# Performance work log

Measured on AMD Instinct MI355X. Metric: run time of the kernel, lower is better.

Reference implementation:

```python
import jax, jax.numpy as jnp
import numpy as np

B, T, C = 4, 2048, 768
H = 12
D = C // H  # head dim 64

def setup_inputs() -> dict:
    key = jax.random.key(0)
    ks = jax.random.split(key, 6)
    scale = 1.0 / np.sqrt(C)
    x = jax.random.normal(ks[0], (B, T, C), dtype=jnp.float32)
    attention_mask = jax.random.randint(ks[1], (B, T), 0, 2, dtype=jnp.int64)
    Wqkv = jax.random.normal(ks[2], (C, 3 * C), dtype=jnp.float32) * scale
    bqkv = jax.random.normal(ks[3], (3 * C,), dtype=jnp.float32) * 0.02
    Wo = jax.random.normal(ks[4], (C, C), dtype=jnp.float32) * scale
    bo = jax.random.normal(ks[5], (C,), dtype=jnp.float32) * 0.02
    return {"x": x, "attention_mask": attention_mask, "Wqkv": Wqkv,
            "bqkv": bqkv, "Wo": Wo, "bo": bo}

def reference(x, attention_mask, Wqkv, bqkv, Wo, bo):
    # fused QKV projection: [B,T,3C]
    qkv = jnp.einsum('btc,cd->btd', x, Wqkv) + bqkv
    q, k, v = jnp.split(qkv, 3, axis=-1)
    # reshape to [B,H,T,D]
    q = q.reshape(B, T, H, D).transpose(0, 2, 1, 3)
    k = k.reshape(B, T, H, D).transpose(0, 2, 1, 3)
    v = v.reshape(B, T, H, D).transpose(0, 2, 1, 3)
    # module quirk: True (attended) where attention_mask == 0
    keep = (attention_mask == 0)[:, None, None, :]  # [B,1,1,T]
    scores = jnp.einsum('bhqd,bhkd->bhqk', q, k) / np.sqrt(D)
    scores = jnp.where(keep, scores, jnp.finfo(scores.dtype).min)
    probs = jax.nn.softmax(scores, axis=-1)
    context = jnp.einsum('bhqk,bhkd->bhqd', probs, v)
    context = context.transpose(0, 2, 1, 3).reshape(B, T, C)
    return jnp.einsum('btc,cd->btd', context, Wo) + bo
```

## Files before the change

### kernel.cpp

```cpp
#include <hip/hip_runtime.h>
#include <stdint.h>

#define AS1 __attribute__((address_space(1)))
#define AS3 __attribute__((address_space(3)))

typedef _Float16 f16;
typedef _Float16 f16x8 __attribute__((ext_vector_type(8)));
typedef _Float16 f16x4 __attribute__((ext_vector_type(4)));
typedef _Float16 f16x2 __attribute__((ext_vector_type(2)));
typedef float    f32x4  __attribute__((ext_vector_type(4)));
typedef float    f32x16 __attribute__((ext_vector_type(16)));
typedef uint32_t u32x4  __attribute__((ext_vector_type(4)));
typedef uint32_t u32x2  __attribute__((ext_vector_type(2)));

#define B_  4
#define T_  2048
#define C_  768
#define H_  12
#define D_  64
#define M_  (B_*T_)
#define N1_ (3*C_)

__device__ __forceinline__ void g2l16(const void* g, void* l) {
  __builtin_amdgcn_global_load_lds((const AS1 void*)g, (AS3 void*)l, 16, 0, 0);
}

__device__ __forceinline__ f32x4 fzero4() { f32x4 z = {0.f, 0.f, 0.f, 0.f}; return z; }

__device__ __forceinline__ uint32_t pk_u32(float a, float b) {
  auto t = __builtin_amdgcn_cvt_pkrtz(a, b);
  return *(uint32_t*)&t;
}

__device__ __forceinline__ void pl32swap(uint32_t& d, uint32_t& s) {
  u32x2 r = __builtin_amdgcn_permlane32_swap(d, s, false, false);
  d = r[0]; s = r[1];
}

__global__ __launch_bounds__(256)
void transpose_cvt_k(const float* __restrict__ in, f16* __restrict__ out, int R, int C) {
  __shared__ float tile[32][33];
  const int tx = threadIdx.x & 31, ty = threadIdx.x >> 5;
  const int c0 = blockIdx.x * 32, r0 = blockIdx.y * 32;
#pragma unroll
  for (int i = 0; i < 32; i += 8)
    tile[ty + i][tx] = in[(long)(r0 + ty + i) * C + c0 + tx];
  __syncthreads();
#pragma unroll
  for (int i = 0; i < 32; i += 8)
    out[(long)(c0 + ty + i) * R + r0 + tx] = (f16)tile[tx][ty + i];
}

__global__ __launch_bounds__(256)
void convert_f32_f16(const float* __restrict__ in, f16* __restrict__ out) {
  const int i = (blockIdx.x * 256 + threadIdx.x) * 4;
  const float4 v = *(const float4*)(in + i);
  f16x4 o = {(f16)v.x, (f16)v.y, (f16)v.z, (f16)v.w};
  *(f16x4*)(out + i) = o;
}

__global__ __launch_bounds__(256)
void init_idx_kernel(int* __restrict__ idx, int* __restrict__ cnt) {
  const int g = blockIdx.x * 256 + threadIdx.x;
  idx[g] = 0;
  if (g < B_) cnt[g] = 0;
}

__global__ __launch_bounds__(256)
void compact_kernel(const int* __restrict__ mask, int* __restrict__ idx,
                    int* __restrict__ cnt) {
  const int b = blockIdx.y;
  const int t = blockIdx.x * 256 + threadIdx.x;
  if (mask[b * T_ + t] == 0) {
    const int s = atomicAdd(&cnt[b], 1);
    idx[b * T_ + s] = t;
  }
}

__global__ __launch_bounds__(256)
void build_vt(const f16* __restrict__ Vc, const int* __restrict__ cnt,
              f16* __restrict__ vt) {
  __shared__ f16 tile[32][33];
  const int z = blockIdx.z, b = z / H_, h = z % H_;
  const int s0 = blockIdx.x * 32, d0 = blockIdx.y * 32;
  if (s0 >= ((cnt[b] + 63) & ~63)) return;
  const int tx = threadIdx.x & 31, ty = threadIdx.x >> 5;
  f16* dst = vt + (long)z * D_ * T_;
#pragma unroll
  for (int i = 0; i < 32; i += 8)
    tile[ty + i][tx] = Vc[(long)(b * T_ + s0 + ty + i) * C_ + h * D_ + d0 + tx];
  __syncthreads();
#pragma unroll
  for (int i = 0; i < 32; i += 8)
    dst[(long)(d0 + ty + i) * T_ + s0 + tx] = tile[tx][ty + i];
}

template <typename OutT>
__global__ __launch_bounds__(256)
void gemm_bias_kernel(const f16* __restrict__ A, const f16* __restrict__ Bt,
                      const float* __restrict__ bias, OutT* __restrict__ Cc,
                      int K, int ldc) {
  __shared__ f16 lA[128 * 32];
  __shared__ f16 lB[128 * 32];
  const int tid = threadIdx.x;
  const int n0 = blockIdx.x * 128, m0 = blockIdx.y * 128;
  const int lane = tid & 63, w = tid >> 6;
  const int wm = (w & 1) * 64, wn = (w >> 1) * 64;
  const int r15 = lane & 15, q4 = lane >> 4;

  const int c0 = tid, c1 = 256 + tid;
  const int ar0 = c0 >> 2, ak0 = (c0 & 3) * 8;
  const int ar1 = c1 >> 2, ak1 = (c1 & 3) * 8;
  const f16* Ab = A + (long)m0 * K;
  const f16* Bb = Bt + (long)n0 * K;

  f32x4 acc[4][4];
#pragma unroll
  for (int i = 0; i < 4; i++)
#pragma unroll
    for (int j = 0; j < 4; j++) acc[i][j] = fzero4();

  for (int kb = 0; kb < K; kb += 32) {
    g2l16(Ab + (long)ar0 * K + kb + ak0, &lA[c0 * 8]);
    g2l16(Ab + (long)ar1 * K + kb + ak1, &lA[c1 * 8]);
    g2l16(Bb + (long)ar0 * K + kb + ak0, &lB[c0 * 8]);
    g2l16(Bb + (long)ar1 * K + kb + ak1, &lB[c1 * 8]);
    __syncthreads();
    f16x8 af[4], bfv[4];
#pragma unroll
    for (int mi = 0; mi < 4; mi++)
      af[mi] = *(const f16x8*)&lA[(wm + mi * 16 + r15) * 32 + q4 * 8];
#pragma unroll
    for (int ni = 0; ni < 4; ni++)
      bfv[ni] = *(const f16x8*)&lB[(wn + ni * 16 + r15) * 32 + q4 * 8];
#pragma unroll
    for (int mi = 0; mi < 4; mi++)
#pragma unroll
      for (int ni = 0; ni < 4; ni++)
        acc[mi][ni] = __builtin_amdgcn_mfma_f32_16x16x32_f16(af[mi], bfv[ni], acc[mi][ni], 0, 0, 0);
    __syncthreads();
  }

#pragma unroll
  for (int ni = 0; ni < 4; ni++) {
    const int col = n0 + wn + ni * 16 + r15;
    const float bs = bias[col];
#pragma unroll
    for (int mi = 0; mi < 4; mi++) {
#pragma unroll
      for (int r = 0; r < 4; r++) {
        const int row = m0 + wm + mi * 16 + q4 * 4 + r;
        Cc[(long)row * ldc + col] = (OutT)(acc[mi][ni][r] + bs);
      }
    }
  }
}

__global__ __launch_bounds__(512, 2)
void gemm_qkv256(const f16* __restrict__ A, const f16* __restrict__ Bt,
                 const float* __restrict__ bias, f16* __restrict__ Qb,
                 f16* __restrict__ Kc, f16* __restrict__ Vc,
                 const int* __restrict__ idx, const int* __restrict__ cnt) {
  const int K = C_;
  __shared__ f16 lA[2 * 256 * 64];
  __shared__ f16 lB[2 * 256 * 64];
  const int tid = threadIdx.x;
  const int nb = blockIdx.x;
  const int mb = blockIdx.y;
  const bool isQ = nb < 3;

  int b = 0, s0 = 0;
  if (!isQ) {
    b = mb >> 3;
    s0 = (mb & 7) * 256;
    if (s0 >= cnt[b]) return;
  }

  const int lane = tid & 63, w = tid >> 6;
  const int wmi = w >> 2, wni = w & 3;
  const int r15 = lane & 15, q4 = lane >> 4;
  const int rx = (r15 & 7) * 8;

  const int trow = tid >> 3;
  const int koffsw = (((tid & 7) ^ (trow & 7)) * 8);
  const f16* pA[4];
  const f16* pB[4];
#pragma unroll
  for (int i = 0; i < 4; i++) {
    const int ri = i * 64 + trow;
    long grow;
    if (isQ) grow = (long)mb * 256 + ri;
    else     grow = (long)b * T_ + idx[b * T_ + s0 + ri];
    pA[i] = A + grow * K + koffsw;
    pB[i] = Bt + (long)(nb * 256 + ri) * K + koffsw;
  }
  const int lofs = tid * 8;

  f32x4 acc[8][4];
#pragma unroll
  for (int i = 0; i < 8; i++)
#pragma unroll
    for (int j = 0; j < 4; j++) acc[i][j] = fzero4();

#define STAGE_QKV(bufsel, kb) do {                                        \
  const int lb = (bufsel) * 16384;                                        \
  _Pragma("unroll")                                                       \
  for (int i = 0; i < 4; i++) {                                           \
    g2l16(pA[i] + (kb), &lA[lb + i * 4096 + lofs]);                       \
    g2l16(pB[i] + (kb), &lB[lb + i * 4096 + lofs]);                       \
  }                                                                       \
} while (0)

#define COMPUTE_QKV(bufsel) do {                                          \
  const int lb = (bufsel) * 16384;                                        \
  _Pragma("unroll")                                                       \
  for (int kh = 0; kh < 2; kh++) {                                        \
    const int cofs = (kh * 32 + q4 * 8) ^ rx;                             \
    f16x8 af[8], bf[4];                                                   \
    _Pragma("unroll")                                                     \
    for (int mi = 0; mi < 8; mi++)                                        \
      af[mi] = *(const f16x8*)&lA[lb + (wmi * 128 + mi * 16 + r15) * 64 + cofs]; \
    _Pragma("unroll")                                                     \
    for (int ni = 0; ni < 4; ni++)                                        \
      bf[ni] = *(const f16x8*)&lB[lb + (wni * 64 + ni * 16 + r15) * 64 + cofs];  \
    _Pragma("unroll")                                                     \
    for (int mi = 0; mi < 8; mi++)                                        \
      _Pragma("unroll")                                                   \
      for (int ni = 0; ni < 4; ni++)                                      \
        acc[mi][ni] = __builtin_amdgcn_mfma_f32_16x16x32_f16(af[mi], bf[ni], acc[mi][ni], 0, 0, 0); \
  }                                                                       \
} while (0)

  STAGE_QKV(0, 0);
  __syncthreads();

  int cur = 0;
  const int NT = K / 64;
  for (int t = 0; t < NT - 1; t++) {
    STAGE_QKV(cur ^ 1, (t + 1) * 64);
    COMPUTE_QKV(cur);
    __syncthreads();
    cur ^= 1;
  }
  COMPUTE_QKV(cur);

#undef STAGE_QKV
#undef COMPUTE_QKV

#pragma unroll
  for (int ni = 0; ni < 4; ni++) {
    const int cN = nb * 256 + wni * 64 + ni * 16 + r15;
    const float bs = bias[cN];
    f16* outp;
    int ocol;
    long rowbase;
    if (isQ)               { outp = Qb; ocol = cN;        rowbase = (long)mb * 256; }
    else if (cN < 2 * C_)  { outp = Kc; ocol = cN - C_;   rowbase = (long)b * T_ + s0; }
    else                   { outp = Vc; ocol = cN - 2*C_; rowbase = (long)b * T_ + s0; }
#pragma unroll
    for (int mi = 0; mi < 8; mi++) {
#pragma unroll
      for (int r = 0; r < 4; r++) {
        const long row = rowbase + wmi * 128 + mi * 16 + q4 * 4 + r;
        outp[row * C_ + ocol] = (f16)(acc[mi][ni][r] + bs);
      }
    }
  }
}

__global__ __launch_bounds__(256, 4)
void attn_kernel(const f16* __restrict__ Qb, const f16* __restrict__ Kc,
                 const f16* __restrict__ vtc, const int* __restrict__ cnt,
                 f16* __restrict__ ctx) {
  __shared__ f16 Ks[2][64 * 64];
  __shared__ f16 Vs[2][64 * 64];
  __shared__ float Ls[4][32];
  const int tid = threadIdx.x, lane = tid & 63, w = tid >> 6;
  const int l31 = lane & 31, hh = lane >> 5;

  const int g = blockIdx.y * 16 + blockIdx.x;
  const int xcd = g & 7, local = g >> 3;
  const int bh = xcd * 6 + (local >> 4);
  const int q0 = (local & 15) * 128;
  const int b = bh / H_, h = bh % H_;

  const f16* Qg = Qb + (long)(b * T_ + q0) * C_ + h * D_;
  const f16* Kbase = Kc + (long)b * T_ * C_ + h * D_;
  const f16* Vg = vtc + (long)bh * D_ * T_;
  const int nk = cnt[b];
  const int nkt = (nk + 63) >> 6;

  const f16 qsc = (f16)0.18033688f;
  f16x8 bq[4];
#pragma unroll
  for (int j = 0; j < 4; j++) {
    f16x8 v = *(const f16x8*)(Qg + (long)(w * 32 + l31) * C_ + j * 16 + hh * 8);
#pragma unroll
    for (int e = 0; e < 8; e++) v[e] = v[e] * qsc;
    bq[j] = v;
  }

  const int r_0 = w * 16 + (lane >> 3);
  const int sc = ((lane & 7) ^ (r_0 & 7)) * 8;
  const f16* Ksrc0 = Kbase + (long)r_0 * C_ + sc;
  const f16* Ksrc1 = Kbase + (long)(r_0 + 8) * C_ + sc;
  const f16* Vsrc0 = Vg + (long)r_0 * T_ + sc;
  const f16* Vsrc1 = Vg + (long)(r_0 + 8) * T_ + sc;
  const int ld0 = w * 1024 + lane * 8;
  const int ld1 = ld0 + 512;

#define ATTN_STAGE(bs, kt) do {                                  \
    g2l16(Ksrc0 + (long)(kt) * C_, &Ks[bs][ld0]);                \
    g2l16(Ksrc1 + (long)(kt) * C_, &Ks[bs][ld1]);                \
    g2l16(Vsrc0 + (kt), &Vs[bs][ld0]);                           \
    g2l16(Vsrc1 + (kt), &Vs[bs][ld1]);                           \
  } while (0)

  float l_acc = 0.f;
  f32x16 O[2];
#pragma unroll
  for (int dt = 0; dt < 2; dt++)
#pragma unroll
    for (int r = 0; r < 16; r++) O[dt][r] = 0.f;

  const int swz = l31 & 7;

  ATTN_STAGE(0, 0);
  __syncthreads();

  int cur = 0;
  for (int t = 0; t < nkt; t++) {
    const int kt = t * 64;
    if (t + 1 < nkt) ATTN_STAGE(cur ^ 1, kt + 64);

    u32x4 paw[4];
    const bool full = (kt + 64 <= nk);
#pragma unroll
    for (int t2 = 0; t2 < 2; t2++) {
      f32x16 acc;
      if (full) {
#pragma unroll
        for (int r = 0; r < 16; r++) acc[r] = 0.f;
      } else {
        const int kbase = kt + t2 * 32 + hh * 4;
#pragma unroll
        for (int g4 = 0; g4 < 4; g4++)
#pragma unroll
          for (int i = 0; i < 4; i++)
            acc[4 * g4 + i] = (kbase + 8 * g4 + i < nk) ? 0.f : -1e30f;
      }
#pragma unroll
      for (int j = 0; j < 4; j++) {
        f16x8 ak = *(const f16x8*)&Ks[cur][(t2 * 32 + l31) * 64 + (((j * 2 + hh) ^ swz) << 3)];
        acc = __builtin_amdgcn_mfma_f32_32x32x16_f16(ak, bq[j], acc, 0, 0, 0);
      }
      uint32_t wg[4], xg[4];
#pragma unroll
      for (int g4 = 0; g4 < 4; g4++) {
        const float p0 = __builtin_amdgcn_exp2f(acc[4 * g4 + 0]);
        const float p1 = __builtin_amdgcn_exp2f(acc[4 * g4 + 1]);
        const float p2 = __builtin_amdgcn_exp2f(acc[4 * g4 + 2]);
        const float p3 = __builtin_amdgcn_exp2f(acc[4 * g4 + 3]);
        l_acc += (p0 + p1) + (p2 + p3);
        wg[g4] = pk_u32(p0, p1);
        xg[g4] = pk_u32(p2, p3);
      }
#pragma unroll
      for (int jl = 0; jl < 2; jl++) {
        uint32_t w0 = wg[2 * jl], w2v = wg[2 * jl + 1];
        uint32_t w1 = xg[2 * jl], w3v = xg[2 * jl + 1];
        pl32swap(w0, w2v);
        pl32swap(w1, w3v);
        paw[2 * t2 + jl][0] = w0;  paw[2 * t2 + jl][1] = w1;
        paw[2 * t2 + jl][2] = w2v; paw[2 * t2 + jl][3] = w3v;
      }
    }

#pragma unroll
    for (int j = 0; j < 4; j++) {
      const f16x8 pa = *(const f16x8*)&paw[j];
#pragma unroll
      for (int dt = 0; dt < 2; dt++) {
        const int vrow = dt * 32 + l31;
        f16x8 vb = *(const f16x8*)&Vs[cur][vrow * 64 + (((j * 2 + hh) ^ swz) << 3)];
        O[dt] = __builtin_amdgcn_mfma_f32_32x32x16_f16(pa, vb, O[dt], 0, 0, 0);
      }
    }

    __syncthreads();
    cur ^= 1;
  }
#undef ATTN_STAGE

  l_acc += __shfl_xor(l_acc, 32);
  asm volatile("s_waitcnt lgkmcnt(0)" ::: "memory");
  if (hh == 0) Ls[w][l31] = l_acc;
  asm volatile("s_waitcnt lgkmcnt(0)" ::: "memory");
#pragma unroll
  for (int g4 = 0; g4 < 4; g4++) {
    const f32x4 lv = *(const f32x4*)&Ls[w][g4 * 8 + hh * 4];
#pragma unroll
    for (int i = 0; i < 4; i++) {
      const float inv = 1.f / lv[i];
      const int row = b * T_ + q0 + w * 32 + g4 * 8 + hh * 4 + i;
#pragma unroll
      for (int dt = 0; dt < 2; dt++)
        ctx[(long)row * C_ + h * D_ + dt * 32 + l31] = (f16)(O[dt][4 * g4 + i] * inv);
    }
  }
}

extern "C" void kernel_launch(void* const* d_in, const int* in_sizes, int n_in,
                              void* d_out, int out_size, void* d_ws, size_t ws_size,
                              hipStream_t stream) {
  (void)in_sizes; (void)n_in; (void)out_size; (void)ws_size;
  const float* x    = (const float*)d_in[0];
  const int*   mask = (const int*)  d_in[1];
  const float* Wqkv = (const float*)d_in[2];
  const float* bqkv = (const float*)d_in[3];
  const float* Wo   = (const float*)d_in[4];
  const float* bo   = (const float*)d_in[5];
  float* out = (float*)d_out;

  char* ws = (char*)d_ws;
  const size_t OFF_WQKVT = 0;
  const size_t OFF_WOT   = OFF_WQKVT + 3538944;
  const size_t OFF_Q     = OFF_WOT + 1179648;
  const size_t OFF_KC    = OFF_Q + 12582912;
  const size_t OFF_VC    = OFF_KC + 12582912;
  const size_t OFF_VT    = OFF_VC + 12582912;
  const size_t OFF_XH    = OFF_VT + 12582912;
  const size_t OFF_IDX   = OFF_XH + 12582912;
  const size_t OFF_CNT   = OFF_IDX + 32768;
  f16* WqkvT = (f16*)(ws + OFF_WQKVT);
  f16* WoT   = (f16*)(ws + OFF_WOT);
  f16* Qb    = (f16*)(ws + OFF_Q);
  f16* Kc    = (f16*)(ws + OFF_KC);
  f16* Vc    = (f16*)(ws + OFF_VC);
  f16* Vtc   = (f16*)(ws + OFF_VT);
  f16* xh    = (f16*)(ws + OFF_XH);
  f16* ctx   = (f16*)(ws + OFF_XH);
  int* idx   = (int*)(ws + OFF_IDX);
  int* cnt   = (int*)(ws + OFF_CNT);

  transpose_cvt_k<<<dim3(72, 24), 256, 0, stream>>>(Wqkv, WqkvT, 768, 2304);
  transpose_cvt_k<<<dim3(24, 24), 256, 0, stream>>>(Wo, WoT, 768, 768);
  convert_f32_f16<<<dim3(M_ * C_ / 1024), 256, 0, stream>>>(x, xh);
  init_idx_kernel<<<dim3(B_ * T_ / 256), 256, 0, stream>>>(idx, cnt);
  compact_kernel<<<dim3(T_ / 256, B_), 256, 0, stream>>>(mask, idx, cnt);
  gemm_qkv256<<<dim3(9, 32), 512, 0, stream>>>(xh, WqkvT, bqkv, Qb, Kc, Vc, idx, cnt);
  build_vt<<<dim3(64, 2, 48), 256, 0, stream>>>(Vc, cnt, Vtc);
  attn_kernel<<<dim3(16, 48), 256, 0, stream>>>(Qb, Kc, Vtc, cnt, ctx);
  gemm_bias_kernel<float><<<dim3(6, 64), 256, 0, stream>>>(ctx, WoT, bo, out, 768, 768);
}
```

Before: 195.3 us.

## Fuse prep kernels, write transposed V from QKV GEMM, add MFMA priority hints

Merges the weight transposes, the x conversion and the index init into a single prep launch, removing several kernel launches. The QKV GEMM epilogue now writes V directly in the per-head transposed layout, which drops the separate build_vt pass and its extra round-trip through global memory. It also wraps the attention MFMA blocks with s_setprio to favour the matrix instructions. The strided 8-byte transposed stores in the GEMM epilogue may coalesce poorly, and the padded tail region of Vt is no longer written by a separate pass.

```diff
diff --git a/kernel.cpp b/kernel.cpp
--- a/kernel.cpp
+++ b/kernel.cpp
@@ -38,32 +38,35 @@
 }
 
 __global__ __launch_bounds__(256)
-void transpose_cvt_k(const float* __restrict__ in, f16* __restrict__ out, int R, int C) {
+void prep_kernel(const float* __restrict__ Wqkv, f16* __restrict__ WqkvT,
+                 const float* __restrict__ Wo, f16* __restrict__ WoT,
+                 const float* __restrict__ x, f16* __restrict__ xh,
+                 int* __restrict__ idx, int* __restrict__ cnt) {
   __shared__ float tile[32][33];
-  const int tx = threadIdx.x & 31, ty = threadIdx.x >> 5;
-  const int c0 = blockIdx.x * 32, r0 = blockIdx.y * 32;
-#pragma unroll
-  for (int i = 0; i < 32; i += 8)
-    tile[ty + i][tx] = in[(long)(r0 + ty + i) * C + c0 + tx];
-  __syncthreads();
-#pragma unroll
-  for (int i = 0; i < 32; i += 8)
-    out[(long)(c0 + ty + i) * R + r0 + tx] = (f16)tile[tx][ty + i];
-}
-
-__global__ __launch_bounds__(256)
-void convert_f32_f16(const float* __restrict__ in, f16* __restrict__ out) {
-  const int i = (blockIdx.x * 256 + threadIdx.x) * 4;
-  const float4 v = *(const float4*)(in + i);
-  f16x4 o = {(f16)v.x, (f16)v.y, (f16)v.z, (f16)v.w};
-  *(f16x4*)(out + i) = o;
-}
-
-__global__ __launch_bounds__(256)
-void init_idx_kernel(int* __restrict__ idx, int* __restrict__ cnt) {
-  const int g = blockIdx.x * 256 + threadIdx.x;
-  idx[g] = 0;
-  if (g < B_) cnt[g] = 0;
+  const int blk = blockIdx.x;
+  if (blk < 2304) {
+    const float* in; f16* out; int R, C, bx, by;
+    if (blk < 1728) { in = Wqkv; out = WqkvT; R = 768; C = 2304; bx = blk % 72; by = blk / 72; }
+    else { const int k = blk - 1728; in = Wo; out = WoT; R = 768; C = 768; bx = k % 24; by = k / 24; }
+    const int tx = threadIdx.x & 31, ty = threadIdx.x >> 5;
+    const int c0 = bx * 32, r0 = by * 32;
+#pragma unroll
+    for (int i = 0; i < 32; i += 8)
+      tile[ty + i][tx] = in[(long)(r0 + ty + i) * C + c0 + tx];
+    __syncthreads();
+#pragma unroll
+    for (int i = 0; i < 32; i += 8)
+      out[(long)(c0 + ty + i) * R + r0 + tx] = (f16)tile[tx][ty + i];
+  } else if (blk < 8448) {
+    const int i = ((blk - 2304) * 256 + threadIdx.x) * 4;
+    const float4 v = *(const float4*)(x + i);
+    f16x4 o = {(f16)v.x, (f16)v.y, (f16)v.z, (f16)v.w};
+    *(f16x4*)(xh + i) = o;
+  } else {
+    const int g = (blk - 8448) * 256 + threadIdx.x;
+    idx[g] = 0;
+    if (g < B_) cnt[g] = 0;
+  }
 }
 
 __global__ __launch_bounds__(256)
@@ -75,24 +78,6 @@
     const int s = atomicAdd(&cnt[b], 1);
     idx[b * T_ + s] = t;
   }
-}
-
-__global__ __launch_bounds__(256)
-void build_vt(const f16* __restrict__ Vc, const int* __restrict__ cnt,
-              f16* __restrict__ vt) {
-  __shared__ f16 tile[32][33];
-  const int z = blockIdx.z, b = z / H_, h = z % H_;
-  const int s0 = blockIdx.x * 32, d0 = blockIdx.y * 32;
-  if (s0 >= ((cnt[b] + 63) & ~63)) return;
-  const int tx = threadIdx.x & 31, ty = threadIdx.x >> 5;
-  f16* dst = vt + (long)z * D_ * T_;
-#pragma unroll
-  for (int i = 0; i < 32; i += 8)
-    tile[ty + i][tx] = Vc[(long)(b * T_ + s0 + ty + i) * C_ + h * D_ + d0 + tx];
-  __syncthreads();
-#pragma unroll
-  for (int i = 0; i < 32; i += 8)
-    dst[(long)(d0 + ty + i) * T_ + s0 + tx] = tile[tx][ty + i];
 }
 
 template <typename OutT>
@@ -159,7 +144,7 @@
 __global__ __launch_bounds__(512, 2)
 void gemm_qkv256(const f16* __restrict__ A, const f16* __restrict__ Bt,
                  const float* __restrict__ bias, f16* __restrict__ Qb,
-                 f16* __restrict__ Kc, f16* __restrict__ Vc,
+                 f16* __restrict__ Kc, f16* __restrict__ Vt,
                  const int* __restrict__ idx, const int* __restrict__ cnt) {
   const int K = C_;
   __shared__ f16 lA[2 * 256 * 64];
@@ -251,18 +236,34 @@
   for (int ni = 0; ni < 4; ni++) {
     const int cN = nb * 256 + wni * 64 + ni * 16 + r15;
     const float bs = bias[cN];
-    f16* outp;
-    int ocol;
-    long rowbase;
-    if (isQ)               { outp = Qb; ocol = cN;        rowbase = (long)mb * 256; }
-    else if (cN < 2 * C_)  { outp = Kc; ocol = cN - C_;   rowbase = (long)b * T_ + s0; }
-    else                   { outp = Vc; ocol = cN - 2*C_; rowbase = (long)b * T_ + s0; }
-#pragma unroll
-    for (int mi = 0; mi < 8; mi++) {
-#pragma unroll
-      for (int r = 0; r < 4; r++) {
-        const long row = rowbase + wmi * 128 + mi * 16 + q4 * 4 + r;
-        outp[row * C_ + ocol] = (f16)(acc[mi][ni][r] + bs);
+    if (isQ) {
+#pragma unroll
+      for (int mi = 0; mi < 8; mi++)
+#pragma unroll
+        for (int r = 0; r < 4; r++) {
+          const long row = (long)mb * 256 + wmi * 128 + mi * 16 + q4 * 4 + r;
+          Qb[row * C_ + cN] = (f16)(acc[mi][ni][r] + bs);
+        }
+    } else if (cN < 2 * C_) {
+      const int ocol = cN - C_;
+#pragma unroll
+      for (int mi = 0; mi < 8; mi++)
+#pragma unroll
+        for (int r = 0; r < 4; r++) {
+          const long row = (long)b * T_ + s0 + wmi * 128 + mi * 16 + q4 * 4 + r;
+          Kc[row * C_ + ocol] = (f16)(acc[mi][ni][r] + bs);
+        }
+    } else {
+      const int vcol = cN - 2 * C_;
+      const int vh = vcol >> 6, d = vcol & 63;
+      f16* dst = Vt + ((long)(b * H_ + vh) * D_ + d) * T_;
+#pragma unroll
+      for (int mi = 0; mi < 8; mi++) {
+        const long slot = s0 + wmi * 128 + mi * 16 + q4 * 4;
+        f16x4 v4;
+#pragma unroll
+        for (int r = 0; r < 4; r++) v4[r] = (f16)(acc[mi][ni][r] + bs);
+        *(f16x4*)&dst[slot] = v4;
       }
     }
   }
@@ -349,11 +350,13 @@
           for (int i = 0; i < 4; i++)
             acc[4 * g4 + i] = (kbase + 8 * g4 + i < nk) ? 0.f : -1e30f;
       }
+      __builtin_amdgcn_s_setprio(1);
 #pragma unroll
       for (int j = 0; j < 4; j++) {
         f16x8 ak = *(const f16x8*)&Ks[cur][(t2 * 32 + l31) * 64 + (((j * 2 + hh) ^ swz) << 3)];
         acc = __builtin_amdgcn_mfma_f32_32x32x16_f16(ak, bq[j], acc, 0, 0, 0);
       }
+      __builtin_amdgcn_s_setprio(0);
       uint32_t wg[4], xg[4];
 #pragma unroll
       for (int g4 = 0; g4 < 4; g4++) {
@@ -376,6 +379,7 @@
       }
     }
 
+    __builtin_amdgcn_s_setprio(1);
 #pragma unroll
     for (int j = 0; j < 4; j++) {
       const f16x8 pa = *(const f16x8*)&paw[j];
@@ -386,6 +390,7 @@
         O[dt] = __builtin_amdgcn_mfma_f32_32x32x16_f16(pa, vb, O[dt], 0, 0, 0);
       }
     }
+    __builtin_amdgcn_s_setprio(0);
 
     __syncthreads();
     cur ^= 1;
@@ -427,8 +432,7 @@
   const size_t OFF_WOT   = OFF_WQKVT + 3538944;
   const size_t OFF_Q     = OFF_WOT + 1179648;
   const size_t OFF_KC    = OFF_Q + 12582912;
-  const size_t OFF_VC    = OFF_KC + 12582912;
-  const size_t OFF_VT    = OFF_VC + 12582912;
+  const size_t OFF_VT    = OFF_KC + 12582912;
   const size_t OFF_XH    = OFF_VT + 12582912;
   const size_t OFF_IDX   = OFF_XH + 12582912;
   const size_t OFF_CNT   = OFF_IDX + 32768;
@@ -436,20 +440,15 @@
   f16* WoT   = (f16*)(ws + OFF_WOT);
   f16* Qb    = (f16*)(ws + OFF_Q);
   f16* Kc    = (f16*)(ws + OFF_KC);
-  f16* Vc    = (f16*)(ws + OFF_VC);
   f16* Vtc   = (f16*)(ws + OFF_VT);
   f16* xh    = (f16*)(ws + OFF_XH);
   f16* ctx   = (f16*)(ws + OFF_XH);
   int* idx   = (int*)(ws + OFF_IDX);
   int* cnt   = (int*)(ws + OFF_CNT);
 
-  transpose_cvt_k<<<dim3(72, 24), 256, 0, stream>>>(Wqkv, WqkvT, 768, 2304);
-  transpose_cvt_k<<<dim3(24, 24), 256, 0, stream>>>(Wo, WoT, 768, 768);
-  convert_f32_f16<<<dim3(M_ * C_ / 1024), 256, 0, stream>>>(x, xh);
-  init_idx_kernel<<<dim3(B_ * T_ / 256), 256, 0, stream>>>(idx, cnt);
+  prep_kernel<<<dim3(8480), 256, 0, stream>>>(Wqkv, WqkvT, Wo, WoT, x, xh, idx, cnt);
   compact_kernel<<<dim3(T_ / 256, B_), 256, 0, stream>>>(mask, idx, cnt);
-  gemm_qkv256<<<dim3(9, 32), 512, 0, stream>>>(xh, WqkvT, bqkv, Qb, Kc, Vc, idx, cnt);
-  build_vt<<<dim3(64, 2, 48), 256, 0, stream>>>(Vc, cnt, Vtc);
+  gemm_qkv256<<<dim3(9, 32), 512, 0, stream>>>(xh, WqkvT, bqkv, Qb, Kc, Vtc, idx, cnt);
   attn_kernel<<<dim3(16, 48), 256, 0, stream>>>(Qb, Kc, Vtc, cnt, ctx);
   gemm_bias_kernel<float><<<dim3(6, 64), 256, 0, stream>>>(ctx, WoT, bo, out, 768, 768);
 }
```

Result: faster. 190.4 us (-2.5%).
